# Optimization experiments

Measured on AMD Instinct MI355X. Metric: run time of the kernel, lower is better.

The kernel has to match this reference:

```python
import jax, jax.numpy as jnp
import numpy as np

V, L, H, D = 2048, 16, 8, 64   # vocab, max_chars, n_head, word_vec_d
B = 8192                        # number of words in batch (rows of char_code)
NW_TOTAL = 8192                 # len(word_code)
N_NAMES = 2048                  # total names (4 words each)
N_GROUPS = 8                    # groups of names (256 each)
PAD = 0
TEMP = D ** 0.5
LN_EPS = 1e-5


def make_pos():
    freq = D // 2
    inv = 1.0 / np.power(10000.0, np.arange(freq) / freq)
    ph = np.outer(np.arange(L), inv)
    return jnp.asarray(np.hstack([np.cos(ph), np.sin(ph)]).astype(np.float32))


def setup_inputs() -> dict:
    key = jax.random.key(0)
    ks = jax.random.split(key, 8)
    char_emb = jax.random.normal(ks[0], (V, D), jnp.float32) * 0.02
    char_emb = char_emb.at[PAD].set(0.0)  # padding_idx row
    Wc = jax.random.normal(ks[1], (D, 3 * H * D), jnp.float32) * 0.02
    bc = jnp.zeros((3 * H * D,), jnp.float32)
    Wp = jax.random.normal(ks[2], (D, 3 * H * D), jnp.float32) * 0.02
    bp = jnp.zeros((3 * H * D,), jnp.float32)
    gamma = jnp.ones((D,), jnp.float32)
    beta = jnp.zeros((D,), jnp.float32)
    W1 = jax.random.normal(ks[3], (H, 16), jnp.float32) * 0.1
    b1 = jnp.zeros((16,), jnp.float32)
    W2 = jax.random.normal(ks[4], (16, 8), jnp.float32) * 0.1
    b2 = jnp.zeros((8,), jnp.float32)
    char_code = jax.random.randint(ks[5], (B, L), 1, V)
    char_code = char_code.at[::4, -2:].set(PAD)  # some padded tails
    word_code = jax.random.randint(ks[6], (NW_TOTAL,), 0, B)
    n_words = np.full((N_NAMES,), NW_TOTAL // N_NAMES, dtype=np.int64)
    n_names = np.full((N_GROUPS,), N_NAMES // N_GROUPS, dtype=np.int64)
    return {"char_emb": char_emb, "Wc": Wc, "bc": bc, "Wp": Wp, "bp": bp,
            "gamma": gamma, "beta": beta, "W1": W1, "b1": b1, "W2": W2, "b2": b2,
            "char_code": char_code, "word_code": word_code,
            "n_words": n_words, "n_names": n_names}


def reference(char_emb, Wc, bc, Wp, bp, gamma, beta, W1, b1, W2, b2,
              char_code, word_code, n_words, n_names):
    pos = make_pos()
    # ComputeQKV: linear d -> 3*H*d, reshape [N,3,H,D]
    cqkv = (char_emb @ Wc + bc).reshape(V, 3, H, D)
    cq, ck, cv = cqkv[:, 0], cqkv[:, 1], cqkv[:, 2]        # [V,H,D]
    pqkv = (pos @ Wp + bp).reshape(L, 3, H, D)
    pq, pk, pv = pqkv[:, 0], pqkv[:, 1], pqkv[:, 2]        # [L,H,D]
    # precomputed score tables
    char_qk = jnp.einsum('xhd,yhd->hxy', cq, ck).at[:, :, PAD].set(-1e9)  # [H,V,V]
    pos_qk = jnp.einsum('xhd,yhd->hxy', pq, pk)                            # [H,L,L]
    # char_q@pos_k + (pos_q@char_k)^T summed over the first dim of char_pos_qk
    cp = jnp.einsum('vhd,lhd->hvl', cq, pk) + jnp.einsum('lhd,vhd->hvl', pq, ck)  # [H,V,L]
    code = char_code                                        # [B,L]
    # gather-assembled scores, no [H,B*L,V] intermediate
    sim = (char_qk[:, code[:, :, None], code[:, None, :]]   # [H,B,L,L]
           + cp[:, code]
           + pos_qk[:, None]) / TEMP
    attn = jax.nn.softmax(sim, axis=-1)                     # [H,B,L,L] (dropout=0)
    v = jnp.transpose(cv[code], (2, 0, 1, 3)) + pv.transpose(1, 0, 2)[:, None]  # [H,B,L,D]
    out = jnp.einsum('hbij,hbjd->bihd', attn, v)            # [B,L,H,D]
    mu = out.mean(-1, keepdims=True)
    var = out.var(-1, keepdims=True)
    out = (out - mu) / jnp.sqrt(var + LN_EPS) * gamma + beta  # LayerNorm(D)
    char_ft = jnp.transpose(out, (0, 2, 1, 3))              # [B,H,L,D]
    mask = (code != PAD)
    pooled = jnp.einsum('bl,bhld->bhd', mask.astype(out.dtype), char_ft) \
             / mask.sum(-1)[:, None, None]                  # masked mean over chars
    x = jnp.transpose(pooled, (0, 2, 1))                    # [B,D,H]
    x = jax.nn.relu(x @ W1 + b1) @ W2 + b2                  # MLP over head dim -> [B,D,8]
    word_ft = x.reshape(B, -1)[word_code]                   # [NW_TOTAL, D*8]
    nw = np.asarray(n_words)
    seg = jnp.asarray(np.repeat(np.arange(nw.size), nw))
    name_ft = jax.ops.segment_sum(word_ft, seg, num_segments=nw.size) \
              / jnp.asarray(nw, word_ft.dtype)[:, None]     # ragged mean -> [N_NAMES, D*8]
    splits = np.cumsum(np.asarray(n_names))[:-1]
    return tuple(jnp.split(name_ft, splits, axis=0))
```

## Files before the change

### kernel.cpp

```cpp
#include <hip/hip_runtime.h>
#include <hip/hip_bf16.h>
#include <math.h>

typedef __attribute__((ext_vector_type(8))) short bfrag;
typedef __attribute__((ext_vector_type(4))) float ffrag;
typedef __attribute__((ext_vector_type(4))) float f4v;
typedef __attribute__((ext_vector_type(2))) float f2v;

#define C3 1536
#define PS 24

__device__ __forceinline__ unsigned short f2bf(float f) {
    unsigned u = __float_as_uint(f);
    return (unsigned short)((u + 0x7FFFu + ((u >> 16) & 1u)) >> 16);
}

__device__ __forceinline__ float row16_sum(float x) {
    int v;
    v = __builtin_amdgcn_update_dpp(0, __float_as_int(x), 0xB1, 0xF, 0xF, true);
    x += __int_as_float(v);
    v = __builtin_amdgcn_update_dpp(0, __float_as_int(x), 0x4E, 0xF, 0xF, true);
    x += __int_as_float(v);
    v = __builtin_amdgcn_update_dpp(0, __float_as_int(x), 0x124, 0xF, 0xF, true);
    x += __int_as_float(v);
    v = __builtin_amdgcn_update_dpp(0, __float_as_int(x), 0x128, 0xF, 0xF, true);
    x += __int_as_float(v);
    return x;
}

__global__ __launch_bounds__(256) void precompute_kernel(
    const float* __restrict__ char_emb, const float* __restrict__ Wc, const float* __restrict__ bc,
    const float* __restrict__ Wp, const float* __restrict__ bp,
    const float* __restrict__ gamma, const float* __restrict__ beta,
    unsigned short* __restrict__ cqkv, unsigned short* __restrict__ pbf,
    unsigned short* __restrict__ pvb, float* __restrict__ gbtab)
{
    const int b = blockIdx.x;
    const int t = threadIdx.x;
    if (b < 1536) {
        const int mt = b / 6;
        const int nt = b - mt * 6;
        const int m0 = mt * 8;
        const int c = nt * 256 + t;
        const float qs = (c < 512) ? 0.125f : 1.f;
        const float bias = bc[c];
        float acc[8];
        #pragma unroll
        for (int r = 0; r < 8; ++r) acc[r] = bias;
        #pragma unroll 16
        for (int dd = 0; dd < 64; ++dd) {
            const float wv = Wc[dd * C3 + c];
            #pragma unroll
            for (int r = 0; r < 8; ++r)
                acc[r] = fmaf(char_emb[(m0 + r) * 64 + dd], wv, acc[r]);
        }
        #pragma unroll
        for (int r = 0; r < 8; ++r)
            cqkv[(size_t)(m0 + r) * C3 + c] = f2bf(acc[r] * qs);
    } else {
        const int e = b - 1536;
        const int l = e / 6;
        const int cc = e - l * 6;
        if (b == 1536 && t < 64) {
            #pragma unroll
            for (int dt = 0; dt < 4; ++dt) {
                gbtab[t * 8 + dt]     = gamma[dt * 16 + t];
                gbtab[t * 8 + 4 + dt] = beta[dt * 16 + t];
            }
        }
        __shared__ float spos[64];
        if (t < 64) {
            const int f = t & 31;
            const float inv = exp2f(-(float)f * 0.41524101186092034f);
            const float ph = (float)l * inv;
            spos[t] = (t < 32) ? cosf(ph) : sinf(ph);
        }
        __syncthreads();
        const int c = t + cc * 256;
        float acc = bp[c];
        #pragma unroll
        for (int dd = 0; dd < 64; ++dd)
            acc = fmaf(spos[dd], Wp[dd * C3 + c], acc);
        if (c < 1024) {
            const float qs = (c < 512) ? 0.125f : 1.f;
            pbf[(c >> 6) * 1024 + l * 64 + (c & 63)] = f2bf(acc * qs);
        } else {
            const int h = (c >> 6) & 7, d = c & 63;
            pvb[((h * 4 + (d >> 4)) * 2 + (l >> 3)) * 128 + (d & 15) * 8 + (l & 7)] = f2bf(acc);
        }
    }
}

__global__ __launch_bounds__(256, 4) void attn_kernel(
    const unsigned short* __restrict__ cqkv, const unsigned short* __restrict__ pbf,
    const unsigned short* __restrict__ pvb, const int* __restrict__ char_code,
    const float* __restrict__ gbtab,
    const float* __restrict__ W1, const float* __restrict__ b1,
    const float* __restrict__ W2, const float* __restrict__ b2,
    float* __restrict__ x)
{
    __shared__ __attribute__((aligned(16))) unsigned short sVt[8 * 1024];
    __shared__ __attribute__((aligned(16))) unsigned short sP[8 * 16 * PS];
    __shared__ float sPool[512];
    __shared__ float sHid[64 * 17];
    __shared__ float sWb[280];

    const int t = threadIdx.x;
    const int lane = t & 63;
    const int wid = t >> 6;
    const int w = blockIdx.x;
    const int quad = lane >> 4;
    const int n = lane & 15;
    const int q2 = quad & 1;

    if (t < 128) { sWb[t] = W1[t]; sWb[144 + t] = W2[t]; }
    else if (t < 144) sWb[t] = b1[t - 128];
    else if (t < 152) sWb[272 + (t - 144)] = b2[t - 144];

    const int code = char_code[w * 16 + n];
    const bool kvalid = (code != 0);
    const unsigned long long msk = __ballot(kvalid);
    const int nv = __popcll(msk & 0xFFFFull);

    const f4v g4 = *(const f4v*)(gbtab + n * 8);
    const f4v b4 = *(const f4v*)(gbtab + n * 8 + 4);

    #pragma unroll
    for (int c2 = 0; c2 < 2; ++c2) {
        const int h = wid + c2 * 4;
        unsigned short* vt = sVt + h * 1024;
        const unsigned short* cvp = cqkv + (size_t)code * C3 + 1024 + h * 64;
        #pragma unroll
        for (int cc = 0; cc < 2; ++cc) {
            const int d8 = quad + cc * 4;
            const bfrag cv = *(const bfrag*)(cvp + d8 * 8);
            #pragma unroll
            for (int j = 0; j < 8; ++j) {
                const int d = d8 * 8 + j;
                const int e = ((d >> 4) * 2 + (n >> 3)) * 128
                            + ((d & 15) ^ ((n >> 3) << 2)) * 8 + (n & 7);
                vt[e] = (unsigned short)cv[j];
            }
        }
    }

    ffrag accS[2];
    #pragma unroll
    for (int c2 = 0; c2 < 2; ++c2) { ffrag z = {0.f,0.f,0.f,0.f}; accS[c2] = z; }
    #pragma unroll
    for (int c2 = 0; c2 < 2; ++c2) {
        const int h = wid + c2 * 4;
        const unsigned short* cbase = cqkv + (size_t)code * C3 + h * 64;
        const unsigned short* pq = pbf + h * 1024 + n * 64;
        const unsigned short* pk = pbf + (8 + h) * 1024 + n * 64;
        #pragma unroll
        for (int cc = 0; cc < 2; ++cc) {
            const int off = quad * 8 + cc * 32;
            const bfrag cqF = *(const bfrag*)(cbase + off);
            const bfrag ckF = *(const bfrag*)(cbase + 512 + off);
            const bfrag pqF = *(const bfrag*)(pq + off);
            const bfrag pkF = *(const bfrag*)(pk + off);
            accS[c2] = __builtin_amdgcn_mfma_f32_16x16x32_bf16(cqF, ckF, accS[c2], 0, 0, 0);
            accS[c2] = __builtin_amdgcn_mfma_f32_16x16x32_bf16(cqF, pkF, accS[c2], 0, 0, 0);
            accS[c2] = __builtin_amdgcn_mfma_f32_16x16x32_bf16(ckF, pqF, accS[c2], 0, 0, 0);
            accS[c2] = __builtin_amdgcn_mfma_f32_16x16x32_bf16(pqF, pkF, accS[c2], 0, 0, 0);
        }
    }

    #pragma unroll
    for (int c2 = 0; c2 < 2; ++c2) {
        const int h = wid + c2 * 4;
        unsigned short* pt = sP + h * 16 * PS;
        #pragma unroll
        for (int r = 0; r < 4; ++r) {
            const float pr = kvalid ? __expf(accS[c2][r]) : 0.f;
            pt[(quad * 4 + r) * PS + n] = f2bf(pr);
        }
    }

    bfrag onesf;
    #pragma unroll
    for (int j = 0; j < 8; ++j) onesf[j] = (short)0x3F80;

    #pragma unroll
    for (int c2 = 0; c2 < 2; ++c2) {
        const int h = wid + c2 * 4;
        unsigned short* pt = sP + h * 16 * PS;
        unsigned short* vt = sVt + h * 1024;
        bfrag ap;
        #pragma unroll
        for (int j = 0; j < 8; ++j) ap[j] = 0;
        if (quad < 2) ap = *(const bfrag*)(pt + n * PS + quad * 8);
        ffrag accO[4];
        #pragma unroll
        for (int dt = 0; dt < 4; ++dt) { ffrag z = {0.f,0.f,0.f,0.f}; accO[dt] = z; }
        #pragma unroll
        for (int dt = 0; dt < 4; ++dt) {
            const bfrag bcv = *(const bfrag*)(vt + (dt * 2 + q2) * 128 + (n ^ (q2 << 2)) * 8);
            accO[dt] = __builtin_amdgcn_mfma_f32_16x16x32_bf16(ap, bcv, accO[dt], 0, 0, 0);
            const bfrag bpv = *(const bfrag*)(pvb + ((h * 4 + dt) * 2 + q2) * 128 + n * 8);
            accO[dt] = __builtin_amdgcn_mfma_f32_16x16x32_bf16(ap, bpv, accO[dt], 0, 0, 0);
        }
        ffrag accE = {0.f, 0.f, 0.f, 0.f};
        accE = __builtin_amdgcn_mfma_f32_16x16x32_bf16(ap, onesf, accE, 0, 0, 0);

        float ps1[4], ps2[4];
        #pragma unroll
        for (int r = 0; r < 4; ++r) {
            ps1[r] = accO[0][r] + accO[1][r] + accO[2][r] + accO[3][r];
            ps2[r] = accO[0][r]*accO[0][r] + accO[1][r]*accO[1][r]
                   + accO[2][r]*accO[2][r] + accO[3][r]*accO[3][r];
            ps1[r] = row16_sum(ps1[r]);
            ps2[r] = row16_sum(ps2[r]);
        }
        float pool[4] = {0.f, 0.f, 0.f, 0.f};
        #pragma unroll
        for (int r = 0; r < 4; ++r) {
            const float mu   = ps1[r] * 0.015625f;
            const float var  = fmaxf(ps2[r] * 0.015625f - mu * mu, 0.f);
            const float rstd = rsqrtf(var + accE[r] * accE[r] * 1e-5f);
            const float iv = ((msk >> (quad * 4 + r)) & 1ull) ? 1.f : 0.f;
            #pragma unroll
            for (int dt = 0; dt < 4; ++dt)
                pool[dt] += iv * fmaf((accO[dt][r] - mu) * rstd, g4[dt], b4[dt]);
        }
        #pragma unroll
        for (int xm = 16; xm <= 32; xm <<= 1) {
            #pragma unroll
            for (int dt = 0; dt < 4; ++dt) pool[dt] += __shfl_xor(pool[dt], xm);
        }
        if (quad == 0) {
            const float invnv = 1.f / (float)nv;
            #pragma unroll
            for (int dt = 0; dt < 4; ++dt)
                sPool[h * 64 + n * 4 + dt] = pool[dt] * invnv;
        }
    }
    __syncthreads();

    if (t < 64) {
        const int dmap = (t & 15) * 4 + (t >> 4);
        float pl[8];
        #pragma unroll
        for (int hh = 0; hh < 8; ++hh) pl[hh] = sPool[hh * 64 + dmap];
        #pragma unroll
        for (int c = 0; c < 16; ++c) {
            float hs = sWb[128 + c];
            #pragma unroll
            for (int hh = 0; hh < 8; ++hh) hs = fmaf(pl[hh], sWb[hh * 16 + c], hs);
            sHid[t * 17 + c] = fmaxf(hs, 0.f);
        }
    }
    __syncthreads();
    {
        const int d = t >> 2, o0 = (t & 3) * 2;
        float a0 = sWb[272 + o0], a1 = sWb[272 + o0 + 1];
        #pragma unroll
        for (int c = 0; c < 16; ++c) {
            const float hc = sHid[d * 17 + c];
            a0 = fmaf(hc, sWb[144 + c * 8 + o0], a0);
            a1 = fmaf(hc, sWb[144 + c * 8 + o0 + 1], a1);
        }
        f2v res; res[0] = a0; res[1] = a1;
        *(f2v*)(x + (size_t)w * 512 + t * 2) = res;
    }
}

__global__ __launch_bounds__(256) void name_avg_kernel(
    const float* __restrict__ x, const int* __restrict__ word_code,
    const int* __restrict__ n_words, float* __restrict__ out)
{
    const int t = threadIdx.x;
    const int lane = t & 63;
    const int nm = blockIdx.x * 4 + (t >> 6);

    int part = 0;
    for (int i = lane; i < nm; i += 64) part += n_words[i];
    #pragma unroll
    for (int xm = 1; xm <= 32; xm <<= 1) part += __shfl_xor(part, xm);
    const int off = part;
    const int cnt = n_words[nm];

    f4v a0 = {0.f,0.f,0.f,0.f}, a1 = {0.f,0.f,0.f,0.f};
    for (int r = 0; r < cnt; ++r) {
        const int wc = word_code[off + r];
        const f4v u0 = *(const f4v*)(x + (size_t)wc * 512 + lane * 8);
        const f4v u1 = *(const f4v*)(x + (size_t)wc * 512 + lane * 8 + 4);
        #pragma unroll
        for (int k = 0; k < 4; ++k) { a0[k] += u0[k]; a1[k] += u1[k]; }
    }
    const float inv = 1.f / (float)cnt;
    #pragma unroll
    for (int k = 0; k < 4; ++k) { a0[k] *= inv; a1[k] *= inv; }
    *(f4v*)(out + (size_t)nm * 512 + lane * 8) = a0;
    *(f4v*)(out + (size_t)nm * 512 + lane * 8 + 4) = a1;
}

extern "C" void kernel_launch(void* const* d_in, const int* in_sizes, int n_in,
                              void* d_out, int out_size, void* d_ws, size_t ws_size,
                              hipStream_t stream) {
    (void)in_sizes; (void)n_in; (void)out_size; (void)ws_size;
    const float* char_emb = (const float*)d_in[0];
    const float* Wc    = (const float*)d_in[1];
    const float* bc    = (const float*)d_in[2];
    const float* Wp    = (const float*)d_in[3];
    const float* bp    = (const float*)d_in[4];
    const float* gamma = (const float*)d_in[5];
    const float* beta  = (const float*)d_in[6];
    const float* W1    = (const float*)d_in[7];
    const float* b1    = (const float*)d_in[8];
    const float* W2    = (const float*)d_in[9];
    const float* b2    = (const float*)d_in[10];
    const int* char_code = (const int*)d_in[11];
    const int* word_code = (const int*)d_in[12];
    const int* n_words   = (const int*)d_in[13];

    char* ws = (char*)d_ws;
    unsigned short* cqkv = (unsigned short*)ws;
    unsigned short* pbf  = (unsigned short*)(ws + 6291456);
    unsigned short* pvb  = (unsigned short*)(ws + 6324224);
    float* x     = (float*)(ws + 6340608);
    float* gbtab = (float*)(ws + 23117824);
    float* out = (float*)d_out;

    precompute_kernel<<<1632, 256, 0, stream>>>(char_emb, Wc, bc, Wp, bp, gamma, beta,
                                                cqkv, pbf, pvb, gbtab);
    attn_kernel<<<8192, 256, 0, stream>>>(cqkv, pbf, pvb, char_code, gbtab,
                                          W1, b1, W2, b2, x);
    name_avg_kernel<<<512, 256, 0, stream>>>(x, word_code, n_words, out);
}
```

Measured before the change: 200.9 us.

## Fuse per-head loops and halve LDS buffers to raise attention occupancy

Merges the three separate per-head loops (V transpose, score MFMAs, softmax write and PV) into one loop per head, so each wave reuses a single V and P shared-memory slot instead of holding two heads. This halves the sVt and sP buffers and raises launch bounds from 4 to 8 blocks per CU, aiming for more resident waves to hide gather latency. It serializes the two heads inside each wave, which gives less instruction-level parallelism. Each wave only touches its own slot, so no barriers are needed when a slot is reused.

```diff
diff --git a/kernel.cpp b/kernel.cpp
--- a/kernel.cpp
+++ b/kernel.cpp
@@ -91,7 +91,7 @@
     }
 }
 
-__global__ __launch_bounds__(256, 4) void attn_kernel(
+__global__ __launch_bounds__(256, 8) void attn_kernel(
     const unsigned short* __restrict__ cqkv, const unsigned short* __restrict__ pbf,
     const unsigned short* __restrict__ pvb, const int* __restrict__ char_code,
     const float* __restrict__ gbtab,
@@ -99,8 +99,8 @@
     const float* __restrict__ W2, const float* __restrict__ b2,
     float* __restrict__ x)
 {
-    __shared__ __attribute__((aligned(16))) unsigned short sVt[8 * 1024];
-    __shared__ __attribute__((aligned(16))) unsigned short sP[8 * 16 * PS];
+    __shared__ __attribute__((aligned(16))) unsigned short sVt[4 * 1024];
+    __shared__ __attribute__((aligned(16))) unsigned short sP[4 * 16 * PS];
     __shared__ float sPool[512];
     __shared__ float sHid[64 * 17];
     __shared__ float sWb[280];
@@ -125,10 +125,17 @@
     const f4v g4 = *(const f4v*)(gbtab + n * 8);
     const f4v b4 = *(const f4v*)(gbtab + n * 8 + 4);
 
+    unsigned short* vt = sVt + wid * 1024;
+    unsigned short* pt = sP + wid * 16 * PS;
+
+    bfrag onesf;
+    #pragma unroll
+    for (int j = 0; j < 8; ++j) onesf[j] = (short)0x3F80;
+
     #pragma unroll
     for (int c2 = 0; c2 < 2; ++c2) {
         const int h = wid + c2 * 4;
-        unsigned short* vt = sVt + h * 1024;
+
         const unsigned short* cvp = cqkv + (size_t)code * C3 + 1024 + h * 64;
         #pragma unroll
         for (int cc = 0; cc < 2; ++cc) {
@@ -142,14 +149,8 @@
                 vt[e] = (unsigned short)cv[j];
             }
         }
-    }
-
-    ffrag accS[2];
-    #pragma unroll
-    for (int c2 = 0; c2 < 2; ++c2) { ffrag z = {0.f,0.f,0.f,0.f}; accS[c2] = z; }
-    #pragma unroll
-    for (int c2 = 0; c2 < 2; ++c2) {
-        const int h = wid + c2 * 4;
+
+        ffrag accS = {0.f, 0.f, 0.f, 0.f};
         const unsigned short* cbase = cqkv + (size_t)code * C3 + h * 64;
         const unsigned short* pq = pbf + h * 1024 + n * 64;
         const unsigned short* pk = pbf + (8 + h) * 1024 + n * 64;
@@ -160,33 +161,18 @@
             const bfrag ckF = *(const bfrag*)(cbase + 512 + off);
             const bfrag pqF = *(const bfrag*)(pq + off);
             const bfrag pkF = *(const bfrag*)(pk + off);
-            accS[c2] = __builtin_amdgcn_mfma_f32_16x16x32_bf16(cqF, ckF, accS[c2], 0, 0, 0);
-            accS[c2] = __builtin_amdgcn_mfma_f32_16x16x32_bf16(cqF, pkF, accS[c2], 0, 0, 0);
-            accS[c2] = __builtin_amdgcn_mfma_f32_16x16x32_bf16(ckF, pqF, accS[c2], 0, 0, 0);
-            accS[c2] = __builtin_amdgcn_mfma_f32_16x16x32_bf16(pqF, pkF, accS[c2], 0, 0, 0);
-        }
-    }
-
-    #pragma unroll
-    for (int c2 = 0; c2 < 2; ++c2) {
-        const int h = wid + c2 * 4;
-        unsigned short* pt = sP + h * 16 * PS;
+            accS = __builtin_amdgcn_mfma_f32_16x16x32_bf16(cqF, ckF, accS, 0, 0, 0);
+            accS = __builtin_amdgcn_mfma_f32_16x16x32_bf16(cqF, pkF, accS, 0, 0, 0);
+            accS = __builtin_amdgcn_mfma_f32_16x16x32_bf16(ckF, pqF, accS, 0, 0, 0);
+            accS = __builtin_amdgcn_mfma_f32_16x16x32_bf16(pqF, pkF, accS, 0, 0, 0);
+        }
+
         #pragma unroll
         for (int r = 0; r < 4; ++r) {
-            const float pr = kvalid ? __expf(accS[c2][r]) : 0.f;
+            const float pr = kvalid ? __expf(accS[r]) : 0.f;
             pt[(quad * 4 + r) * PS + n] = f2bf(pr);
         }
-    }
-
-    bfrag onesf;
-    #pragma unroll
-    for (int j = 0; j < 8; ++j) onesf[j] = (short)0x3F80;
-
-    #pragma unroll
-    for (int c2 = 0; c2 < 2; ++c2) {
-        const int h = wid + c2 * 4;
-        unsigned short* pt = sP + h * 16 * PS;
-        unsigned short* vt = sVt + h * 1024;
+
         bfrag ap;
         #pragma unroll
         for (int j = 0; j < 8; ++j) ap[j] = 0;
```

Result: slower. 207.5 us (+3.3%).
